# Performance work log

Measured on AMD Instinct MI355X. Metric: run time of the kernel, lower is better.

Reference implementation:

```python
import jax, jax.numpy as jnp
import numpy as np

D, NH, HD, NL, NP, DFF = 256, 8, 32, 4, 4, 1024
B, LQ = 16, 900
SHAPES = np.array([[100, 100], [50, 50], [25, 25], [13, 13]], dtype=np.int64)
_AREAS = SHAPES[:, 0] * SHAPES[:, 1]
LSI = np.concatenate([[0], np.cumsum(_AREAS)[:-1]]).astype(np.int64)
S = int(_AREAS.sum())  # 13294


def setup_inputs() -> dict:
    key = jax.random.key(0)
    ki = iter(jax.random.split(key, 40))
    def nrm(shape, s=1.0):
        return jax.random.normal(next(ki), shape, jnp.float32) * s
    p = dict(
        tgt=nrm((B, LQ, D)),
        query_pos=nrm((B, LQ, D)) * 0.1,
        reference_points=jax.random.uniform(next(ki), (B, LQ, NL, 2), jnp.float32),
        src=nrm((B, S, D)),
        src_spatial_shapes=SHAPES,
        level_start_index=LSI,
        src_padding_mask=np.zeros((B, S), dtype=bool),
        Wq=nrm((D, D), 0.02), bq=jnp.zeros((D,)),
        Wk=nrm((D, D), 0.02), bk=jnp.zeros((D,)),
        Wv=nrm((D, D), 0.02), bv=jnp.zeros((D,)),
        Wo=nrm((D, D), 0.02), bo=jnp.zeros((D,)),
        g2=jnp.ones((D,)), be2=jnp.zeros((D,)),
        Woff=nrm((D, NH * NL * NP * 2), 0.02),
        boff=jax.random.uniform(next(ki), (NH * NL * NP * 2,), jnp.float32, -0.5, 0.5),
        Waw=nrm((D, NH * NL * NP), 0.02), baw=jnp.zeros((NH * NL * NP,)),
        Wval=nrm((D, D), 0.02), bval=jnp.zeros((D,)),
        Wout=nrm((D, D), 0.02), bout=jnp.zeros((D,)),
        g1=jnp.ones((D,)), be1=jnp.zeros((D,)),
        W1f=nrm((D, DFF), 0.02), b1f=jnp.zeros((DFF,)),
        W2f=nrm((DFF, D), 0.02), b2f=jnp.zeros((D,)),
        g3=jnp.ones((D,)), be3=jnp.zeros((D,)),
    )
    return p


def layernorm(x, g, b):
    m = jnp.mean(x, -1, keepdims=True)
    v = jnp.var(x, -1, keepdims=True)
    return (x - m) * jax.lax.rsqrt(v + 1e-5) * g + b


def reference(tgt, query_pos, reference_points, src, src_spatial_shapes,
              level_start_index, src_padding_mask,
              Wq, bq, Wk, bk, Wv, bv, Wo, bo, g2, be2,
              Woff, boff, Waw, baw, Wval, bval, Wout, bout, g1, be1,
              W1f, b1f, W2f, b2f, g3, be3):
    Bq, Lq, _ = tgt.shape
    # ---- self-attention (q = k = tgt + pos, v = tgt), dropout in eval = identity
    q = tgt + query_pos
    qh = (q @ Wq + bq).reshape(Bq, Lq, NH, HD)
    kh = (q @ Wk + bk).reshape(Bq, Lq, NH, HD)
    vh = (tgt @ Wv + bv).reshape(Bq, Lq, NH, HD)
    att = jax.nn.softmax(jnp.einsum('bqhd,bkhd->bhqk', qh, kh) / np.sqrt(HD), axis=-1)
    sa = jnp.einsum('bhqk,bkhd->bqhd', att, vh).reshape(Bq, Lq, D) @ Wo + bo
    tgt = layernorm(tgt + sa, g2, be2)
    # ---- multi-scale deformable cross-attention
    query = tgt + query_pos
    value = src @ Wval + bval
    value = jnp.where(jnp.asarray(src_padding_mask)[..., None], 0.0, value)
    value = value.reshape(Bq, -1, NH, HD)
    off = (query @ Woff + boff).reshape(Bq, Lq, NH, NL, NP, 2)
    aw = jax.nn.softmax((query @ Waw + baw).reshape(Bq, Lq, NH, NL * NP), axis=-1)
    aw = aw.reshape(Bq, Lq, NH, NL, NP)
    ss = np.asarray(src_spatial_shapes)
    lsi = np.asarray(level_start_index)
    norm = jnp.asarray(ss[:, ::-1].astype(np.float32))  # (W, H) per level
    # sampling locations in [0,1]: [B, Lq, NH, NL, NP, 2]
    loc = reference_points[:, :, None, :, None, :] + off / norm[None, None, None, :, None, :]
    out = jnp.zeros((Bq, NH, Lq, HD), value.dtype)
    for l in range(NL):
        Hc, Wc = int(ss[l, 0]), int(ss[l, 1])
        v2 = value[:, lsi[l]:lsi[l] + Hc * Wc].transpose(0, 2, 1, 3)  # [B, NH, H*W, HD]
        x = loc[:, :, :, l, :, 0] * Wc - 0.5  # [B, Lq, NH, NP] (align_corners=False)
        y = loc[:, :, :, l, :, 1] * Hc - 0.5
        x0 = jnp.floor(x); y0 = jnp.floor(y)
        lx = x - x0; ly = y - y0
        x0i = x0.astype(jnp.int32); y0i = y0.astype(jnp.int32)
        samp = jnp.zeros((Bq, NH, Lq * NP, HD), value.dtype)
        for dy, dx, w in ((0, 0, (1 - ly) * (1 - lx)), (0, 1, (1 - ly) * lx),
                          (1, 0, ly * (1 - lx)), (1, 1, ly * lx)):
            xi = x0i + dx; yi = y0i + dy
            valid = (xi >= 0) & (xi < Wc) & (yi >= 0) & (yi < Hc)  # zero padding
            idx = jnp.clip(yi, 0, Hc - 1) * Wc + jnp.clip(xi, 0, Wc - 1)
            idx2 = idx.transpose(0, 2, 1, 3).reshape(Bq, NH, Lq * NP)
            g = jnp.take_along_axis(v2, idx2[..., None], axis=2)  # [B, NH, Lq*NP, HD]
            wv = (w * valid).transpose(0, 2, 1, 3).reshape(Bq, NH, Lq * NP)
            samp = samp + wv[..., None] * g
        samp = samp.reshape(Bq, NH, Lq, NP, HD)
        out = out + jnp.einsum('bqhp,bhqpd->bhqd', aw[:, :, :, l, :], samp)
    ca = out.transpose(0, 2, 1, 3).reshape(Bq, Lq, D) @ Wout + bout
    tgt = layernorm(tgt + ca, g1, be1)
    # ---- FFN
    ff = jax.nn.relu(tgt @ W1f + b1f) @ W2f + b2f
    return layernorm(tgt + ff, g3, be3)
```

## Files before the change

kernel.cpp:

```cpp
#include <hip/hip_runtime.h>
#include <math.h>

#define DD 256
#define NH 8
#define HD 32
#define NL 4
#define NP 4
#define DFF 1024
#define BB 16
#define LQ 900
#define S_TOT 13294

#define M1   (BB * LQ)
#define MP1  14464
#define MV   (BB * S_TOT)
#define MPV  212736

typedef unsigned short u16;
typedef unsigned int   u32;
typedef __attribute__((ext_vector_type(8))) short s8v;
typedef __attribute__((ext_vector_type(4))) float f32x4;

__constant__ int c_H[NL]    = {100, 50, 25, 13};
__constant__ int c_W[NL]    = {100, 50, 25, 13};
__constant__ int c_base[NL] = {0, 10000, 12500, 13125};

__device__ __forceinline__ float b2f(u16 u) {
    return __uint_as_float(((u32)u) << 16);
}
__device__ __forceinline__ u16 f2b(float f) {
    u32 x = __float_as_uint(f);
    u32 r = x + 0x7fffu + ((x >> 16) & 1u);
    return (u16)(r >> 16);
}
__device__ __forceinline__ u32 pk2(float a, float b) {
    return (u32)f2b(a) | ((u32)f2b(b) << 16);
}
__device__ __forceinline__ void gload16(const u16* g, u16* ldsbase) {
    __builtin_amdgcn_global_load_lds(
        (const __attribute__((address_space(1))) unsigned int*)(const void*)g,
        (__attribute__((address_space(3))) unsigned int*)(void*)ldsbase,
        16, 0, 0);
}

#define OFF_QK   0
#define OFF_V    131072
#define OFF_O    196608
#define OFF_VAL  262144
#define OFF_OUT  327680
#define OFF_OA   393216
#define OFF_F1   491520
#define OFF_F2   753664
#define WTS_TOT  1015808

__global__ __launch_bounds__(256)
void prep_kernel(const float* __restrict__ Wq, const float* __restrict__ Wk,
                 const float* __restrict__ Wv, const float* __restrict__ Wo,
                 const float* __restrict__ Wval, const float* __restrict__ Wout,
                 const float* __restrict__ Woff, const float* __restrict__ Waw,
                 const float* __restrict__ W1f, const float* __restrict__ W2f,
                 const float* __restrict__ pbq, const float* __restrict__ pbk,
                 const float* __restrict__ boff, const float* __restrict__ baw,
                 u16* __restrict__ WTS, float* __restrict__ bqk, float* __restrict__ boa)
{
    int t = blockIdx.x;
    if (t >= 992) {
        if (t == 992) {
            for (int i = threadIdx.x; i < 512; i += 256)
                bqk[i] = (i < 256) ? pbq[i] : pbk[i - 256];
        } else {
            for (int i = threadIdx.x; i < 384; i += 256)
                boa[i] = (i < 256) ? boff[i] : baw[i - 256];
        }
        return;
    }
    const float* src; u16* dst; int K, N, tt;
    if (t < 448) {
        int wsel = t >> 6; tt = t & 63;
        const float* srcs[7] = {Wq, Wk, Wv, Wo, Wval, Wout, Woff};
        const int   offs[7]  = {OFF_QK, OFF_QK + 65536, OFF_V, OFF_O, OFF_VAL, OFF_OUT, OFF_OA};
        src = srcs[wsel]; dst = WTS + offs[wsel]; K = 256; N = 256;
    } else if (t < 480) {
        tt = t - 448; src = Waw; dst = WTS + OFF_OA + 65536; K = 256; N = 128;
    } else if (t < 736) {
        tt = t - 480; src = W1f; dst = WTS + OFF_F1; K = 256; N = 1024;
    } else {
        tt = t - 736; src = W2f; dst = WTS + OFF_F2; K = 1024; N = 256;
    }
    int nt = N / 32;
    int n0 = (tt % nt) * 32, k0 = (tt / nt) * 32;

    __shared__ float tb[32][33];
    int tx = threadIdx.x & 31, ty = threadIdx.x >> 5;
    #pragma unroll
    for (int i = 0; i < 4; ++i) {
        int k = ty + i * 8;
        tb[k][tx] = src[(size_t)(k0 + k) * N + n0 + tx];
    }
    __syncthreads();
    #pragma unroll
    for (int i = 0; i < 4; ++i) {
        int n = ty + i * 8;
        dst[(size_t)(n0 + n) * K + k0 + tx] = f2b(tb[tx][n]);
    }
}

template<int BNT, int AF32, int OUTBF, int RELU>
__global__ __launch_bounds__(256)
void mgemm(const void* __restrict__ Av, const u16* __restrict__ Bt,
           const float* __restrict__ bias, void* __restrict__ Cv,
           int K, int N, int Mreal, const float* __restrict__ pos)
{
    constexpr int MF = (BNT == 128) ? 4 : 2;
    __shared__ u16 Asu[128 * 32];
    __shared__ u16 Bsu[BNT * 32];

    int tid = threadIdx.x;
    int w = tid >> 6, l = tid & 63;
    int mbase = (BNT == 128) ? (w >> 1) * 64 : w * 32;
    int nbase = (BNT == 128) ? (w & 1) * 64 : 0;
    long m0 = (long)blockIdx.y * 128;
    int n0 = blockIdx.x * BNT;

    f32x4 acc[MF][4];
    #pragma unroll
    for (int i = 0; i < MF; ++i)
        #pragma unroll
        for (int j = 0; j < 4; ++j) {
            acc[i][j][0] = 0.f; acc[i][j][1] = 0.f;
            acc[i][j][2] = 0.f; acc[i][j][3] = 0.f;
        }

    int lr = l & 15, lk = (l >> 4) * 8;
    int srow = l >> 2;
    int scol = (l & 3) * 8;

    for (int k0 = 0; k0 < K; k0 += 32) {
        if (BNT == 128) {
            #pragma unroll
            for (int j = 0; j < 2; ++j) {
                int row = w * 32 + j * 16;
                gload16(Bt + (size_t)(n0 + row + srow) * K + k0 + scol, &Bsu[row * 32]);
            }
        } else {
            int row = w * 16;
            gload16(Bt + (size_t)(n0 + row + srow) * K + k0 + scol, &Bsu[row * 32]);
        }
        if (AF32) {
            const float* A = (const float*)Av;
            int c = tid;
            #pragma unroll
            for (int it = 0; it < 4; ++it) {
                int row = c >> 3, col = (c & 7) * 4;
                long gr = m0 + row;
                if (gr >= Mreal) gr = Mreal - 1;
                float4 v = *(const float4*)(A + gr * K + k0 + col);
                if (pos) {
                    float4 p = *(const float4*)(pos + gr * K + k0 + col);
                    v.x += p.x; v.y += p.y; v.z += p.z; v.w += p.w;
                }
                ushort4 o;
                o.x = f2b(v.x); o.y = f2b(v.y); o.z = f2b(v.z); o.w = f2b(v.w);
                ((ushort4*)Asu)[c] = o;
                c += 256;
            }
        } else {
            const u16* A = (const u16*)Av;
            #pragma unroll
            for (int j = 0; j < 2; ++j) {
                int row = w * 32 + j * 16;
                gload16(A + (m0 + row + srow) * (long)K + k0 + scol, &Asu[row * 32]);
            }
        }
        __syncthreads();
        s8v af[MF], bf[4];
        #pragma unroll
        for (int mi = 0; mi < MF; ++mi)
            af[mi] = *(const s8v*)(Asu + (mbase + mi * 16 + lr) * 32 + lk);
        #pragma unroll
        for (int nj = 0; nj < 4; ++nj)
            bf[nj] = *(const s8v*)(Bsu + (nbase + nj * 16 + lr) * 32 + lk);
        #pragma unroll
        for (int mi = 0; mi < MF; ++mi)
            #pragma unroll
            for (int nj = 0; nj < 4; ++nj)
                acc[mi][nj] = __builtin_amdgcn_mfma_f32_16x16x32_bf16(
                    af[mi], bf[nj], acc[mi][nj], 0, 0, 0);
        __syncthreads();
    }

    int lq = l >> 4;
    #pragma unroll
    for (int nj = 0; nj < 4; ++nj) {
        int col = n0 + nbase + nj * 16 + lr;
        float bv = bias[col];
        #pragma unroll
        for (int mi = 0; mi < MF; ++mi) {
            #pragma unroll
            for (int r = 0; r < 4; ++r) {
                long row = m0 + mbase + mi * 16 + lq * 4 + r;
                float v = acc[mi][nj][r] + bv;
                if (RELU) v = fmaxf(v, 0.f);
                if (OUTBF) ((u16*)Cv)[row * N + col] = f2b(v);
                else       ((float*)Cv)[row * N + col] = v;
            }
        }
    }
}

#define QT 64
#define KT2 64
#define KSP 48
#define VSP 40
#define PSP 72
__global__ __launch_bounds__(256)
void mattn(const u16* __restrict__ qk, const u16* __restrict__ vh,
           u16* __restrict__ sa)
{
    __shared__ u16 Ks[KT2][KSP];
    __shared__ u32 Vt32[32][VSP];
    __shared__ u16 Ps[4][16][PSP];

    int tid = threadIdx.x;
    int w = tid >> 6, l = tid & 63;
    int lr = l & 15, hi = l >> 4;
    int b = blockIdx.x >> 3, h = blockIdx.x & 7;
    int q0 = blockIdx.y * QT + w * 16;

    s8v qf;
    {
        s8v raw = *(const s8v*)(qk + ((size_t)(b * LQ + q0 + lr) * 512) + h * HD + hi * 8);
        #pragma unroll
        for (int j = 0; j < 8; ++j)
            raw[j] = (short)f2b(b2f((u16)raw[j]) * 0.17677669529663687f);
        qf = raw;
    }

    f32x4 o0 = {0.f,0.f,0.f,0.f}, o1 = {0.f,0.f,0.f,0.f};
    float lrun[4] = {0.f,0.f,0.f,0.f};

    const u16* kbase = qk + (size_t)b * LQ * 512 + 256 + h * HD;
    const u16* vbase = vh + (size_t)b * LQ * 256 + h * HD;

    int krow = tid >> 2, kc8 = (tid & 3) * 8;
    int k2 = tid & 31, d0 = (tid >> 5) * 4;

    for (int kb = 0; kb < LQ; kb += KT2) {
        int gk = kb + krow;        if (gk >= LQ) gk = LQ - 1;
        int gv0 = kb + 2 * k2;     if (gv0 >= LQ) gv0 = LQ - 1;
        int gv1 = kb + 2 * k2 + 1; if (gv1 >= LQ) gv1 = LQ - 1;
        uint4 kv = *(const uint4*)(kbase + (size_t)gk * 512 + kc8);
        uint2 va = *(const uint2*)(vbase + (size_t)gv0 * 256 + d0);
        uint2 vb = *(const uint2*)(vbase + (size_t)gv1 * 256 + d0);
        __syncthreads();
        *(uint4*)(&Ks[krow][kc8]) = kv;
        Vt32[d0 + 0][k2] = (va.x & 0xffffu)      | (vb.x << 16);
        Vt32[d0 + 1][k2] = (va.x >> 16)          | (vb.x & 0xffff0000u);
        Vt32[d0 + 2][k2] = (va.y & 0xffffu)      | (vb.y << 16);
        Vt32[d0 + 3][k2] = (va.y >> 16)          | (vb.y & 0xffff0000u);
        __syncthreads();

        f32x4 s[4];
        #pragma unroll
        for (int kk = 0; kk < 4; ++kk) {
            s8v bk = *(const s8v*)(&Ks[kk * 16 + lr][hi * 8]);
            f32x4 z = {0.f,0.f,0.f,0.f};
            s[kk] = __builtin_amdgcn_mfma_f32_16x16x32_bf16(qf, bk, z, 0, 0, 0);
        }
        if (kb + KT2 > LQ) {
            #pragma unroll
            for (int kk = 0; kk < 4; ++kk)
                if (kb + kk * 16 + lr >= LQ) {
                    s[kk][0] = -1e30f; s[kk][1] = -1e30f;
                    s[kk][2] = -1e30f; s[kk][3] = -1e30f;
                }
        }

        #pragma unroll
        for (int r = 0; r < 4; ++r) {
            float p0 = __expf(s[0][r]);
            float p1 = __expf(s[1][r]);
            float p2 = __expf(s[2][r]);
            float p3 = __expf(s[3][r]);
            lrun[r] += (p0 + p1) + (p2 + p3);
            int qr = hi * 4 + r;
            Ps[w][qr][lr]      = f2b(p0);
            Ps[w][qr][16 + lr] = f2b(p1);
            Ps[w][qr][32 + lr] = f2b(p2);
            Ps[w][qr][48 + lr] = f2b(p3);
        }

        s8v ap0  = *(const s8v*)(&Ps[w][lr][hi * 8]);
        s8v ap1  = *(const s8v*)(&Ps[w][lr][32 + hi * 8]);
        s8v bv00 = *(const s8v*)(&Vt32[lr][hi * 4]);
        s8v bv10 = *(const s8v*)(&Vt32[lr][16 + hi * 4]);
        s8v bv01 = *(const s8v*)(&Vt32[16 + lr][hi * 4]);
        s8v bv11 = *(const s8v*)(&Vt32[16 + lr][16 + hi * 4]);
        o0 = __builtin_amdgcn_mfma_f32_16x16x32_bf16(ap0, bv00, o0, 0, 0, 0);
        o0 = __builtin_amdgcn_mfma_f32_16x16x32_bf16(ap1, bv10, o0, 0, 0, 0);
        o1 = __builtin_amdgcn_mfma_f32_16x16x32_bf16(ap0, bv01, o1, 0, 0, 0);
        o1 = __builtin_amdgcn_mfma_f32_16x16x32_bf16(ap1, bv11, o1, 0, 0, 0);
    }

    #pragma unroll
    for (int r = 0; r < 4; ++r) {
        float ps = lrun[r];
        ps += __shfl_xor(ps, 1);
        ps += __shfl_xor(ps, 2);
        ps += __shfl_xor(ps, 4);
        ps += __shfl_xor(ps, 8);
        int q = q0 + hi * 4 + r;
        if (q < LQ) {
            float inv = 1.f / ps;
            u16* op = sa + (size_t)(b * LQ + q) * DD + h * HD;
            op[lr]      = f2b(o0[r] * inv);
            op[16 + lr] = f2b(o1[r] * inv);
        }
    }
}

__global__ __launch_bounds__(256)
void ln_kernel(const float* __restrict__ x, const u16* __restrict__ y,
               const float* __restrict__ g, const float* __restrict__ be,
               float* __restrict__ out, const float* __restrict__ pos,
               u16* __restrict__ bfout, int M)
{
    int wave = threadIdx.x >> 6;
    int lane = threadIdx.x & 63;
    int row = blockIdx.x * 4 + wave;
    if (row >= M) return;
    float4 xv = ((const float4*)(x + (size_t)row * DD))[lane];
    ushort4 yv = ((const ushort4*)(y + (size_t)row * DD))[lane];
    float v[4] = {xv.x + b2f(yv.x), xv.y + b2f(yv.y),
                  xv.z + b2f(yv.z), xv.w + b2f(yv.w)};
    float s = v[0] + v[1] + v[2] + v[3];
    float sq = v[0]*v[0] + v[1]*v[1] + v[2]*v[2] + v[3]*v[3];
    for (int o = 32; o; o >>= 1) {
        s += __shfl_xor(s, o);
        sq += __shfl_xor(sq, o);
    }
    float mean = s * (1.f / DD);
    float var = sq * (1.f / DD) - mean * mean;
    float r = rsqrtf(var + 1e-5f);
    float4 gv = ((const float4*)g)[lane];
    float4 bv = ((const float4*)be)[lane];
    float4 ov;
    ov.x = (v[0] - mean) * r * gv.x + bv.x;
    ov.y = (v[1] - mean) * r * gv.y + bv.y;
    ov.z = (v[2] - mean) * r * gv.z + bv.z;
    ov.w = (v[3] - mean) * r * gv.w + bv.w;
    ((float4*)(out + (size_t)row * DD))[lane] = ov;
    if (bfout) {
        float4 pv = make_float4(0.f, 0.f, 0.f, 0.f);
        if (pos) pv = ((const float4*)(pos + (size_t)row * DD))[lane];
        ushort4 bo;
        bo.x = f2b(ov.x + pv.x); bo.y = f2b(ov.y + pv.y);
        bo.z = f2b(ov.z + pv.z); bo.w = f2b(ov.w + pv.w);
        ((ushort4*)(bfout + (size_t)row * DD))[lane] = bo;
    }
}

__global__ __launch_bounds__(256)
void sample_kernel(const float* __restrict__ offaw, const float* __restrict__ refp,
                   const u16* __restrict__ value, u16* __restrict__ out)
{
    __shared__ float2 sPW[128][4];
    __shared__ float4 sPart[4][64];

    int t = threadIdx.x;
    int bq = blockIdx.x;
    int b = bq / LQ;

    if (t < 128) {
        int pt = t;
        int h = pt >> 4, j = pt & 15, l = j >> 2, p = j & 3;
        const float* row = offaw + (size_t)bq * 384;
        float lg = row[256 + h * 16 + j];
        float mx = lg;
        mx = fmaxf(mx, __shfl_xor(mx, 1));
        mx = fmaxf(mx, __shfl_xor(mx, 2));
        mx = fmaxf(mx, __shfl_xor(mx, 4));
        mx = fmaxf(mx, __shfl_xor(mx, 8));
        float e = __expf(lg - mx);
        float se = e;
        se += __shfl_xor(se, 1);
        se += __shfl_xor(se, 2);
        se += __shfl_xor(se, 4);
        se += __shfl_xor(se, 8);
        float aw = e / se;

        float ox = row[h * 32 + l * 8 + p * 2 + 0];
        float oy = row[h * 32 + l * 8 + p * 2 + 1];
        int Hc = c_H[l], Wc = c_W[l];
        float x = refp[(size_t)bq * 8 + l * 2 + 0] * Wc + ox - 0.5f;
        float y = refp[(size_t)bq * 8 + l * 2 + 1] * Hc + oy - 0.5f;
        float x0f = floorf(x), y0f = floorf(y);
        float lx = x - x0f, ly = y - y0f;
        int x0 = (int)x0f, y0 = (int)y0f;
        int vb = (b * S_TOT + c_base[l]) * 64;
        #pragma unroll
        for (int c = 0; c < 4; ++c) {
            int dy = c >> 1, dx = c & 1;
            int xi = x0 + dx, yi = y0 + dy;
            bool ok = (xi >= 0) & (xi < Wc) & (yi >= 0) & (yi < Hc);
            float wgt = (dy ? ly : 1.f - ly) * (dx ? lx : 1.f - lx) * aw;
            float2 pw;
            pw.x = __int_as_float(ok ? vb + (yi * Wc + xi) * 64 : 0);
            pw.y = ok ? wgt : 0.f;
            sPW[pt][c] = pw;
        }
    }
    __syncthreads();

    {
        int jq = t >> 6, h = (t >> 3) & 7, d4 = t & 7;
        const uint2* v64 = (const uint2*)value;
        int lane = h * 8 + d4;
        float a0 = 0.f, a1 = 0.f, a2 = 0.f, a3 = 0.f;
        #pragma unroll
        for (int jj = 0; jj < 4; ++jj) {
            int pt = h * 16 + jq * 4 + jj;
            float2 pw0 = sPW[pt][0];
            float2 pw1 = sPW[pt][1];
            float2 pw2 = sPW[pt][2];
            float2 pw3 = sPW[pt][3];
            uint2 g0 = v64[__float_as_int(pw0.x) + lane];
            uint2 g1 = v64[__float_as_int(pw1.x) + lane];
            uint2 g2 = v64[__float_as_int(pw2.x) + lane];
            uint2 g3 = v64[__float_as_int(pw3.x) + lane];
            a0 += pw0.y * __uint_as_float(g0.x << 16);
            a1 += pw0.y * __uint_as_float(g0.x & 0xffff0000u);
            a2 += pw0.y * __uint_as_float(g0.y << 16);
            a3 += pw0.y * __uint_as_float(g0.y & 0xffff0000u);
            a0 += pw1.y * __uint_as_float(g1.x << 16);
            a1 += pw1.y * __uint_as_float(g1.x & 0xffff0000u);
            a2 += pw1.y * __uint_as_float(g1.y << 16);
            a3 += pw1.y * __uint_as_float(g1.y & 0xffff0000u);
            a0 += pw2.y * __uint_as_float(g2.x << 16);
            a1 += pw2.y * __uint_as_float(g2.x & 0xffff0000u);
            a2 += pw2.y * __uint_as_float(g2.y << 16);
            a3 += pw2.y * __uint_as_float(g2.y & 0xffff0000u);
            a0 += pw3.y * __uint_as_float(g3.x << 16);
            a1 += pw3.y * __uint_as_float(g3.x & 0xffff0000u);
            a2 += pw3.y * __uint_as_float(g3.y << 16);
            a3 += pw3.y * __uint_as_float(g3.y & 0xffff0000u);
        }
        sPart[jq][h * 8 + d4] = make_float4(a0, a1, a2, a3);
    }
    __syncthreads();

    if (t < 64) {
        float4 p0 = sPart[0][t];
        float4 p1 = sPart[1][t];
        float4 p2 = sPart[2][t];
        float4 p3 = sPart[3][t];
        float a0 = (p0.x + p1.x) + (p2.x + p3.x);
        float a1 = (p0.y + p1.y) + (p2.y + p3.y);
        float a2 = (p0.z + p1.z) + (p2.z + p3.z);
        float a3 = (p0.w + p1.w) + (p2.w + p3.w);
        uint2 o;
        o.x = pk2(a0, a1);
        o.y = pk2(a2, a3);
        *(uint2*)(out + (size_t)bq * DD + t * 4) = o;
    }
}

extern "C" void kernel_launch(void* const* d_in, const int* in_sizes, int n_in,
                              void* d_out, int out_size, void* d_ws, size_t ws_size,
                              hipStream_t stream)
{
    const float* tgt  = (const float*)d_in[0];
    const float* qpos = (const float*)d_in[1];
    const float* refp = (const float*)d_in[2];
    const float* src  = (const float*)d_in[3];
    const float* Wq  = (const float*)d_in[7];
    const float* pbq = (const float*)d_in[8];
    const float* Wk  = (const float*)d_in[9];
    const float* pbk = (const float*)d_in[10];
    const float* Wv  = (const float*)d_in[11];
    const float* pbv = (const float*)d_in[12];
    const float* Wo  = (const float*)d_in[13];
    const float* pbo = (const float*)d_in[14];
    const float* g2  = (const float*)d_in[15];
    const float* be2 = (const float*)d_in[16];
    const float* Woff = (const float*)d_in[17];
    const float* boff = (const float*)d_in[18];
    const float* Waw  = (const float*)d_in[19];
    const float* baw  = (const float*)d_in[20];
    const float* Wval = (const float*)d_in[21];
    const float* bval = (const float*)d_in[22];
    const float* Wout = (const float*)d_in[23];
    const float* bout = (const float*)d_in[24];
    const float* g1   = (const float*)d_in[25];
    const float* be1  = (const float*)d_in[26];
    const float* W1f  = (const float*)d_in[27];
    const float* b1f  = (const float*)d_in[28];
    const float* W2f  = (const float*)d_in[29];
    const float* b2f_ = (const float*)d_in[30];
    const float* g3   = (const float*)d_in[31];
    const float* be3  = (const float*)d_in[32];

    char* base = (char*)d_ws;
    size_t off = 0;
    auto alloc = [&](size_t bytes) -> void* {
        void* p = base + off;
        off = (off + bytes + 255) & ~(size_t)255;
        return p;
    };
    const size_t AB = (size_t)MP1 * DD * sizeof(u16);
    u16* B0  = (u16*)alloc(AB);
    u16* B1  = (u16*)alloc(AB);
    u16* BQK = (u16*)alloc((size_t)MP1 * 512 * sizeof(u16));
    u16* B4  = (u16*)alloc(AB);
    u16* TMPB= (u16*)alloc(AB);
    u16* FFH = (u16*)alloc((size_t)MP1 * DFF * sizeof(u16));
    u16* VAL = (u16*)alloc((size_t)MPV * DD * sizeof(u16));
    float* F0 = (float*)alloc((size_t)MP1 * 384 * sizeof(float));
    float* F2 = (float*)alloc((size_t)MP1 * DD * sizeof(float));
    float* F3 = (float*)alloc((size_t)MP1 * DD * sizeof(float));
    u16* WTS = (u16*)alloc((size_t)WTS_TOT * sizeof(u16));
    float* bqk = (float*)alloc(512 * sizeof(float));
    float* boa = (float*)alloc(384 * sizeof(float));

    dim3 blk(256);

    prep_kernel<<<dim3(994), blk, 0, stream>>>(
        Wq, Wk, Wv, Wo, Wval, Wout, Woff, Waw, W1f, W2f,
        pbq, pbk, boff, baw, WTS, bqk, boa);

    const int MT = MP1 / 128;
    const dim3 gval(2, MPV / 128);
    const dim3 g512b(8,  MT);
    const dim3 g256b(4,  MT);
    const dim3 g384b(6,  MT);
    const dim3 g1kb(16,  MT);

    mgemm<64,1,1,0><<<g512b, blk, 0, stream>>>(tgt, WTS + OFF_QK, bqk, BQK, DD, 512, M1, qpos);
    mgemm<64,1,1,0><<<g256b, blk, 0, stream>>>(tgt, WTS + OFF_V, pbv, B4, DD, DD, M1, nullptr);
    mattn<<<dim3(BB * NH, (LQ + QT - 1) / QT), blk, 0, stream>>>(BQK, B4, B0);
    mgemm<64,0,1,0><<<g256b, blk, 0, stream>>>(B0, WTS + OFF_O, pbo, TMPB, DD, DD, M1, nullptr);
    ln_kernel<<<dim3(M1 / 4), blk, 0, stream>>>(tgt, TMPB, g2, be2, F2, qpos, B1, M1);

    mgemm<128,1,1,0><<<gval, blk, 0, stream>>>(src, WTS + OFF_VAL, bval, VAL, DD, DD, MV, nullptr);
    mgemm<64,0,0,0><<<g384b, blk, 0, stream>>>(B1, WTS + OFF_OA, boa, F0, DD, 384, M1, nullptr);
    sample_kernel<<<dim3(M1), blk, 0, stream>>>(F0, refp, VAL, B4);
    mgemm<64,0,1,0><<<g256b, blk, 0, stream>>>(B4, WTS + OFF_OUT, bout, TMPB, DD, DD, M1, nullptr);
    ln_kernel<<<dim3(M1 / 4), blk, 0, stream>>>(F2, TMPB, g1, be1, F3, nullptr, B1, M1);

    mgemm<64,0,1,1><<<g1kb, blk, 0, stream>>>(B1, WTS + OFF_F1, b1f, FFH, DD, DFF, M1, nullptr);
    mgemm<64,0,1,0><<<g256b, blk, 0, stream>>>(FFH, WTS + OFF_F2, b2f_, TMPB, DFF, DD, M1, nullptr);
    ln_kernel<<<dim3(M1 / 4), blk, 0, stream>>>(F3, TMPB, g3, be3, (float*)d_out, nullptr, nullptr, M1);
}
```

Measured before the change: 385.8 us.

## Pre-convert tgt to bf16 once and double-buffer the value-projection GEMM

A new conversion kernel writes bf16 copies of tgt+query_pos and tgt a single time. The QK and V GEMMs then load bf16 tiles directly instead of each re-reading and converting fp32 inputs. The large value-projection GEMM over src gets a dedicated kernel with double-buffered shared memory, prefetching the next fp32 A tile into registers while MFMAs run on the current one. This costs one extra launch and an extra bf16 round trip through memory, and the dedicated kernel uses twice the LDS, which may lower occupancy.

```diff
diff --git a/kernel.cpp b/kernel.cpp
--- a/kernel.cpp
+++ b/kernel.cpp
@@ -105,11 +105,34 @@
     }
 }
 
-template<int BNT, int AF32, int OUTBF, int RELU>
 __global__ __launch_bounds__(256)
-void mgemm(const void* __restrict__ Av, const u16* __restrict__ Bt,
+void acvt2_kernel(const float* __restrict__ tgt, const float* __restrict__ qpos,
+                  u16* __restrict__ B0, u16* __restrict__ B1)
+{
+    int i8 = blockIdx.x * 256 + threadIdx.x;
+    int row = i8 >> 5;
+    uint4 o0, o1;
+    if (row < M1) {
+        const float4* tp = (const float4*)(tgt + (size_t)i8 * 8);
+        const float4* pp = (const float4*)(qpos + (size_t)i8 * 8);
+        float4 t0 = tp[0], t1 = tp[1], p0 = pp[0], p1 = pp[1];
+        o1.x = pk2(t0.x, t0.y); o1.y = pk2(t0.z, t0.w);
+        o1.z = pk2(t1.x, t1.y); o1.w = pk2(t1.z, t1.w);
+        o0.x = pk2(t0.x + p0.x, t0.y + p0.y); o0.y = pk2(t0.z + p0.z, t0.w + p0.w);
+        o0.z = pk2(t1.x + p1.x, t1.y + p1.y); o0.w = pk2(t1.z + p1.z, t1.w + p1.w);
+    } else {
+        o0.x = o0.y = o0.z = o0.w = 0;
+        o1 = o0;
+    }
+    ((uint4*)B0)[i8] = o0;
+    ((uint4*)B1)[i8] = o1;
+}
+
+template<int BNT, int OUTBF, int RELU>
+__global__ __launch_bounds__(256)
+void mgemm(const u16* __restrict__ A, const u16* __restrict__ Bt,
            const float* __restrict__ bias, void* __restrict__ Cv,
-           int K, int N, int Mreal, const float* __restrict__ pos)
+           int K, int N, int Mreal)
 {
     constexpr int MF = (BNT == 128) ? 4 : 2;
     __shared__ u16 Asu[128 * 32];
@@ -146,31 +169,10 @@
             int row = w * 16;
             gload16(Bt + (size_t)(n0 + row + srow) * K + k0 + scol, &Bsu[row * 32]);
         }
-        if (AF32) {
-            const float* A = (const float*)Av;
-            int c = tid;
-            #pragma unroll
-            for (int it = 0; it < 4; ++it) {
-                int row = c >> 3, col = (c & 7) * 4;
-                long gr = m0 + row;
-                if (gr >= Mreal) gr = Mreal - 1;
-                float4 v = *(const float4*)(A + gr * K + k0 + col);
-                if (pos) {
-                    float4 p = *(const float4*)(pos + gr * K + k0 + col);
-                    v.x += p.x; v.y += p.y; v.z += p.z; v.w += p.w;
-                }
-                ushort4 o;
-                o.x = f2b(v.x); o.y = f2b(v.y); o.z = f2b(v.z); o.w = f2b(v.w);
-                ((ushort4*)Asu)[c] = o;
-                c += 256;
-            }
-        } else {
-            const u16* A = (const u16*)Av;
-            #pragma unroll
-            for (int j = 0; j < 2; ++j) {
-                int row = w * 32 + j * 16;
-                gload16(A + (m0 + row + srow) * (long)K + k0 + scol, &Asu[row * 32]);
-            }
+        #pragma unroll
+        for (int j = 0; j < 2; ++j) {
+            int row = w * 32 + j * 16;
+            gload16(A + (m0 + row + srow) * (long)K + k0 + scol, &Asu[row * 32]);
         }
         __syncthreads();
         s8v af[MF], bf[4];
@@ -203,6 +205,118 @@
                 if (RELU) v = fmaxf(v, 0.f);
                 if (OUTBF) ((u16*)Cv)[row * N + col] = f2b(v);
                 else       ((float*)Cv)[row * N + col] = v;
+            }
+        }
+    }
+}
+
+__global__ __launch_bounds__(256)
+void vgemm(const float* __restrict__ A, const u16* __restrict__ Bt,
+           const float* __restrict__ bias, u16* __restrict__ C, int Mreal)
+{
+    const int K = 256, N = 256;
+    __shared__ u16 Asu[2][128 * 32];
+    __shared__ u16 Bsu[2][128 * 32];
+
+    int tid = threadIdx.x;
+    int w = tid >> 6, l = tid & 63;
+    int wr = w >> 1, wc = w & 1;
+    long m0 = (long)blockIdx.y * 128;
+    int n0 = blockIdx.x * 128;
+    int lr = l & 15, lk = (l >> 4) * 8;
+    int srow = l >> 2, scol = (l & 3) * 8;
+
+    f32x4 acc[4][4];
+    #pragma unroll
+    for (int i = 0; i < 4; ++i)
+        #pragma unroll
+        for (int j = 0; j < 4; ++j) {
+            acc[i][j][0] = 0.f; acc[i][j][1] = 0.f;
+            acc[i][j][2] = 0.f; acc[i][j][3] = 0.f;
+        }
+
+    float4 pref[4];
+
+    #pragma unroll
+    for (int j = 0; j < 2; ++j) {
+        int row = w * 32 + j * 16;
+        gload16(Bt + (size_t)(n0 + row + srow) * K + scol, &Bsu[0][row * 32]);
+    }
+    #pragma unroll
+    for (int it = 0; it < 4; ++it) {
+        int c = tid + it * 256;
+        int row = c >> 3, col = (c & 7) * 4;
+        long gr = m0 + row;
+        if (gr >= Mreal) gr = Mreal - 1;
+        pref[it] = *(const float4*)(A + gr * K + col);
+    }
+    #pragma unroll
+    for (int it = 0; it < 4; ++it) {
+        int c = tid + it * 256;
+        ushort4 o;
+        o.x = f2b(pref[it].x); o.y = f2b(pref[it].y);
+        o.z = f2b(pref[it].z); o.w = f2b(pref[it].w);
+        ((ushort4*)Asu[0])[c] = o;
+    }
+    __syncthreads();
+
+    int cur = 0;
+    for (int s = 0; s < 8; ++s) {
+        int nxt = cur ^ 1;
+        if (s < 7) {
+            int k0 = (s + 1) * 32;
+            #pragma unroll
+            for (int j = 0; j < 2; ++j) {
+                int row = w * 32 + j * 16;
+                gload16(Bt + (size_t)(n0 + row + srow) * K + k0 + scol, &Bsu[nxt][row * 32]);
+            }
+            #pragma unroll
+            for (int it = 0; it < 4; ++it) {
+                int c = tid + it * 256;
+                int row = c >> 3, col = (c & 7) * 4;
+                long gr = m0 + row;
+                if (gr >= Mreal) gr = Mreal - 1;
+                pref[it] = *(const float4*)(A + gr * K + k0 + col);
+            }
+        }
+        s8v af[4], bf[4];
+        #pragma unroll
+        for (int mi = 0; mi < 4; ++mi)
+            af[mi] = *(const s8v*)(Asu[cur] + (wr * 64 + mi * 16 + lr) * 32 + lk);
+        #pragma unroll
+        for (int nj = 0; nj < 4; ++nj)
+            bf[nj] = *(const s8v*)(Bsu[cur] + (wc * 64 + nj * 16 + lr) * 32 + lk);
+        #pragma unroll
+        for (int mi = 0; mi < 4; ++mi)
+            #pragma unroll
+            for (int nj = 0; nj < 4; ++nj)
+                acc[mi][nj] = __builtin_amdgcn_mfma_f32_16x16x32_bf16(
+                    af[mi], bf[nj], acc[mi][nj], 0, 0, 0);
+        if (s < 7) {
+            #pragma unroll
+            for (int it = 0; it < 4; ++it) {
+                int c = tid + it * 256;
+                ushort4 o;
+                o.x = f2b(pref[it].x); o.y = f2b(pref[it].y);
+                o.z = f2b(pref[it].z); o.w = f2b(pref[it].w);
+                ((ushort4*)Asu[nxt])[c] = o;
+            }
+        }
+        __syncthreads();
+        cur = nxt;
+    }
+
+    int lq = l >> 4;
+    #pragma unroll
+    for (int nj = 0; nj < 4; ++nj) {
+        int col = n0 + wc * 64 + nj * 16 + lr;
+        float bv = bias[col];
+        #pragma unroll
+        for (int mi = 0; mi < 4; ++mi) {
+            #pragma unroll
+            for (int r = 0; r < 4; ++r) {
+                long row = m0 + wr * 64 + mi * 16 + lq * 4 + r;
+                C[row * N + col] = f2b(acc[mi][nj][r] + bv);
             }
         }
     }
@@ -535,19 +649,20 @@
     const dim3 g384b(6,  MT);
     const dim3 g1kb(16,  MT);
 
-    mgemm<64,1,1,0><<<g512b, blk, 0, stream>>>(tgt, WTS + OFF_QK, bqk, BQK, DD, 512, M1, qpos);
-    mgemm<64,1,1,0><<<g256b, blk, 0, stream>>>(tgt, WTS + OFF_V, pbv, B4, DD, DD, M1, nullptr);
+    acvt2_kernel<<<dim3(MP1 * 32 / 256), blk, 0, stream>>>(tgt, qpos, B0, B1);
+    mgemm<64,1,0><<<g512b, blk, 0, stream>>>(B0, WTS + OFF_QK, bqk, BQK, DD, 512, M1);
+    mgemm<64,1,0><<<g256b, blk, 0, stream>>>(B1, WTS + OFF_V, pbv, B4, DD, DD, M1);
     mattn<<<dim3(BB * NH, (LQ + QT - 1) / QT), blk, 0, stream>>>(BQK, B4, B0);
-    mgemm<64,0,1,0><<<g256b, blk, 0, stream>>>(B0, WTS + OFF_O, pbo, TMPB, DD, DD, M1, nullptr);
+    mgemm<64,1,0><<<g256b, blk, 0, stream>>>(B0, WTS + OFF_O, pbo, TMPB, DD, DD, M1);
     ln_kernel<<<dim3(M1 / 4), blk, 0, stream>>>(tgt, TMPB, g2, be2, F2, qpos, B1, M1);
 
-    mgemm<128,1,1,0><<<gval, blk, 0, stream>>>(src, WTS + OFF_VAL, bval, VAL, DD, DD, MV, nullptr);
-    mgemm<64,0,0,0><<<g384b, blk, 0, stream>>>(B1, WTS + OFF_OA, boa, F0, DD, 384, M1, nullptr);
+    vgemm<<<gval, blk, 0, stream>>>(src, WTS + OFF_VAL, bval, VAL, MV);
+    mgemm<64,0,0><<<g384b, blk, 0, stream>>>(B1, WTS + OFF_OA, boa, F0, DD, 384, M1);
     sample_kernel<<<dim3(M1), blk, 0, stream>>>(F0, refp, VAL, B4);
-    mgemm<64,0,1,0><<<g256b, blk, 0, stream>>>(B4, WTS + OFF_OUT, bout, TMPB, DD, DD, M1, nullptr);
+    mgemm<64,1,0><<<g256b, blk, 0, stream>>>(B4, WTS + OFF_OUT, bout, TMPB, DD, DD, M1);
     ln_kernel<<<dim3(M1 / 4), blk, 0, stream>>>(F2, TMPB, g1, be1, F3, nullptr, B1, M1);
 
-    mgemm<64,0,1,1><<<g1kb, blk, 0, stream>>>(B1, WTS + OFF_F1, b1f, FFH, DD, DFF, M1, nullptr);
-    mgemm<64,0,1,0><<<g256b, blk, 0, stream>>>(FFH, WTS + OFF_F2, b2f_, TMPB, DFF, DD, M1, nullptr);
+    mgemm<64,1,1><<<g1kb, blk, 0, stream>>>(B1, WTS + OFF_F1, b1f, FFH, DD, DFF, M1);
+    mgemm<64,1,0><<<g256b, blk, 0, stream>>>(FFH, WTS + OFF_F2, b2f_, TMPB, DFF, DD, M1);
     ln_kernel<<<dim3(M1 / 4), blk, 0, stream>>>(F3, TMPB, g3, be3, (float*)d_out, nullptr, nullptr, M1);
 }
```

After: 381.2 us. No clear change (-1.2%).
